# Kernel tuning notes

Measured on AMD Instinct MI355X. Metric: run time of the kernel, lower is better.

## Reference

```python
import jax, jax.numpy as jnp
import numpy as np

N_NODES = 100000
N_EDGES = 1600000
IN_SIZE = 128
HIDDEN = 32
OUT_SIZE = 16


def _mean_agg(h, src, dst, n_nodes):
    # segment-sum of source features into destination nodes, then divide by in-degree
    summed = jax.ops.segment_sum(h[src], dst, num_segments=n_nodes)  # [N, D]
    deg = jax.ops.segment_sum(jnp.ones((src.shape[0],), h.dtype), dst, num_segments=n_nodes)
    return summed / jnp.maximum(deg, 1.0)[:, None]


def _sage_layer(h, src, dst, W_self, W_neigh, b):
    # DGL SAGEConv (mean): fc_self(h) + fc_neigh(mean_neigh(h)) + bias
    agg = _mean_agg(h, src, dst, h.shape[0])
    return h @ W_self + agg @ W_neigh + b


def setup_inputs() -> dict:
    key = jax.random.key(0)
    ks = jax.random.split(key, 9)
    inp = {
        "x": jax.random.normal(ks[0], (N_NODES, IN_SIZE), jnp.float32),
        "edge_src": jax.random.randint(ks[1], (N_EDGES,), 0, N_NODES, jnp.int32),
        "edge_dst": jax.random.randint(ks[2], (N_EDGES,), 0, N_NODES, jnp.int32),
        "W_self1": jax.random.normal(ks[3], (IN_SIZE, HIDDEN), jnp.float32) / np.sqrt(IN_SIZE),
        "W_neigh1": jax.random.normal(ks[4], (IN_SIZE, HIDDEN), jnp.float32) / np.sqrt(IN_SIZE),
        "b1": jnp.zeros((HIDDEN,), jnp.float32),
        "W_self2": jax.random.normal(ks[5], (HIDDEN, HIDDEN), jnp.float32) / np.sqrt(HIDDEN),
        "W_neigh2": jax.random.normal(ks[6], (HIDDEN, HIDDEN), jnp.float32) / np.sqrt(HIDDEN),
        "b2": jnp.zeros((HIDDEN,), jnp.float32),
        "W_self3": jax.random.normal(ks[7], (HIDDEN, OUT_SIZE), jnp.float32) / np.sqrt(HIDDEN),
        "W_neigh3": jax.random.normal(ks[8], (HIDDEN, OUT_SIZE), jnp.float32) / np.sqrt(HIDDEN),
        "b3": jnp.zeros((OUT_SIZE,), jnp.float32),
    }
    return inp


def reference(x, edge_src, edge_dst,
              W_self1, W_neigh1, b1,
              W_self2, W_neigh2, b2,
              W_self3, W_neigh3, b3):
    h = jax.nn.relu(_sage_layer(x, edge_src, edge_dst, W_self1, W_neigh1, b1))
    h = jax.nn.relu(_sage_layer(h, edge_src, edge_dst, W_self2, W_neigh2, b2))
    h = _sage_layer(h, edge_src, edge_dst, W_self3, W_neigh3, b3)
    return h
```

## Files before the change

### kernel.cpp

```cpp
#include <hip/hip_runtime.h>


#define BLOCK 256
#define NBLK 256
#define BSH 9
#define CAP 12288

__global__ void hist_kernel(const int* __restrict__ dst, int* __restrict__ hist,
                            int n_edges, int nbuk, int ch) {
    __shared__ int cnt[256];
    int tid = threadIdx.x;
    for (int i = tid; i < nbuk; i += BLOCK) cnt[i] = 0;
    __syncthreads();
    int e0 = blockIdx.x * ch;
    int e1 = e0 + ch; if (e1 > n_edges) e1 = n_edges;
    for (int e = e0 + tid; e < e1; e += BLOCK)
        atomicAdd(&cnt[dst[e] >> BSH], 1);
    __syncthreads();
    for (int i = tid; i < nbuk; i += BLOCK)
        hist[i * NBLK + blockIdx.x] = cnt[i];
}

__global__ void scanBlk_kernel(int* __restrict__ hist, int* __restrict__ buktot) {
    int b = blockIdx.x;
    int tid = threadIdx.x;
    int orig = hist[b * NBLK + tid];
    int v = orig;
    int lane = tid & 63, w = tid >> 6;
#pragma unroll
    for (int off = 1; off < 64; off <<= 1) {
        int u = __shfl_up(v, off);
        if (lane >= off) v += u;
    }
    __shared__ int wps[4];
    if (lane == 63) wps[w] = v;
    __syncthreads();
    int wadd = 0;
    for (int k = 0; k < w; ++k) wadd += wps[k];
    int excl = v - orig + wadd;
    hist[b * NBLK + tid] = excl;
    if (tid == 255) buktot[b] = excl + orig;
}

__global__ void scanBuk_kernel(const int* __restrict__ buktot, int* __restrict__ bukoff,
                               int nbuk, int* __restrict__ startp, int n_nodes, int n_edges) {
    int tid = threadIdx.x;
    int orig = (tid < nbuk) ? buktot[tid] : 0;
    int v = orig;
    int lane = tid & 63, w = tid >> 6;
#pragma unroll
    for (int off = 1; off < 64; off <<= 1) {
        int u = __shfl_up(v, off);
        if (lane >= off) v += u;
    }
    __shared__ int wps[4];
    if (lane == 63) wps[w] = v;
    __syncthreads();
    int wadd = 0;
    for (int k = 0; k < w; ++k) wadd += wps[k];
    int excl = v - orig + wadd;
    if (tid < nbuk) bukoff[tid] = excl;
    if (tid == 0) { bukoff[nbuk] = n_edges; startp[n_nodes] = n_edges; }
}

__global__ void part_kernel(const int* __restrict__ src, const int* __restrict__ dst,
                            const int* __restrict__ hist, const int* __restrict__ bukoff,
                            int2* __restrict__ pairs, int n_edges, int nbuk, int ch) {
    __shared__ int base[256];
    __shared__ int cnt[256];
    int tid = threadIdx.x;
    for (int i = tid; i < nbuk; i += BLOCK) {
        base[i] = hist[i * NBLK + blockIdx.x] + bukoff[i];
        cnt[i] = 0;
    }
    __syncthreads();
    int e0 = blockIdx.x * ch;
    int e1 = e0 + ch; if (e1 > n_edges) e1 = n_edges;
    for (int e = e0 + tid; e < e1; e += BLOCK) {
        int d = dst[e];
        int b = d >> BSH;
        int r = atomicAdd(&cnt[b], 1);
        pairs[base[b] + r] = make_int2(src[e], d);
    }
}

__global__ void build_kernel(const int2* __restrict__ pairs, const int* __restrict__ bukoff,
                             int* __restrict__ start, float* __restrict__ invdeg,
                             int* __restrict__ csr_src, int n_nodes) {
    __shared__ int deg[512];
    __shared__ int lst[512];
    __shared__ int cur[512];
    __shared__ int wps[4];
    __shared__ int scsr[CAP];

    int b = blockIdx.x;
    int tid = threadIdx.x;
    int e0 = bukoff[b];
    int e1 = bukoff[b + 1];
    int lo = b << BSH;
    int hi = lo + (1 << BSH); if (hi > n_nodes) hi = n_nodes;
    int nn = hi - lo;
    int ne = e1 - e0;

    for (int i = tid; i < 512; i += BLOCK) deg[i] = 0;
    __syncthreads();
    for (int i = e0 + tid; i < e1; i += BLOCK)
        atomicAdd(&deg[pairs[i].y - lo], 1);
    __syncthreads();

    int d0 = deg[2 * tid], d1 = deg[2 * tid + 1];
    int s = d0 + d1;
    int lane = tid & 63, w = tid >> 6;
    int v = s;
#pragma unroll
    for (int off = 1; off < 64; off <<= 1) {
        int u = __shfl_up(v, off);
        if (lane >= off) v += u;
    }
    if (lane == 63) wps[w] = v;
    __syncthreads();
    int wb = 0;
    for (int k = 0; k < w; ++k) wb += wps[k];
    int excl = wb + v - s;
    lst[2 * tid] = excl;
    lst[2 * tid + 1] = excl + d0;
    cur[2 * tid] = 0;
    cur[2 * tid + 1] = 0;
    __syncthreads();

    for (int i = tid; i < nn; i += BLOCK) {
        start[lo + i] = e0 + lst[i];
        int d = deg[i];
        invdeg[lo + i] = 1.0f / (float)(d < 1 ? 1 : d);
    }

    if (ne <= CAP) {
        for (int i = e0 + tid; i < e1; i += BLOCK) {
            int2 pr = pairs[i];
            int dl = pr.y - lo;
            int sl = lst[dl] + atomicAdd(&cur[dl], 1);
            scsr[sl] = pr.x;
        }
        __syncthreads();
        for (int i = tid; i < ne; i += BLOCK) csr_src[e0 + i] = scsr[i];
    } else {
        for (int i = e0 + tid; i < e1; i += BLOCK) {
            int2 pr = pairs[i];
            int dl = pr.y - lo;
            int sl = lst[dl] + atomicAdd(&cur[dl], 1);
            csr_src[e0 + sl] = pr.x;
        }
    }
}

template<int DIN, int DOUT, int OPT, int NPT>
__global__ __launch_bounds__(256, 4)
void proj_reg(const float* __restrict__ h,
              const float* __restrict__ Ws,
              const float* __restrict__ Wn,
              const float* __restrict__ bias,
              float* __restrict__ pre,
              float* __restrict__ p,
              int n_nodes) {
    constexpr int OD  = 2 * DOUT;
    constexpr int OG  = OD / OPT;
    constexpr int NG  = 256 / OG;
    constexpr int NT  = NPT * NG;
    constexpr int NV  = OPT / 4;

    __shared__ float sW[DIN][OD];
    __shared__ float sb[DOUT];

    const int tid = threadIdx.x;
    for (int i = tid; i < DIN * OD; i += 256) {
        int k = i / OD, o = i % OD;
        sW[k][o] = (o < DOUT) ? Ws[k * DOUT + o] : Wn[k * DOUT + (o - DOUT)];
    }
    if (tid < DOUT) sb[tid] = bias[tid];
    __syncthreads();

    const int to = tid % OG;
    const int tn = tid / OG;
    const int o0 = to * OPT;
    const int node0 = blockIdx.x * NT + tn * NPT;

    const float4* __restrict__ xp[NPT];
#pragma unroll
    for (int n = 0; n < NPT; ++n) {
        int node = node0 + n;
        int safe = (node < n_nodes) ? node : (n_nodes - 1);
        xp[n] = reinterpret_cast<const float4*>(h + (size_t)safe * DIN);
    }

    float acc[NPT][OPT];
#pragma unroll
    for (int n = 0; n < NPT; ++n)
#pragma unroll
        for (int o = 0; o < OPT; ++o) acc[n][o] = 0.f;

#pragma unroll 2
    for (int k4 = 0; k4 < DIN / 4; ++k4) {
        float4 xv[NPT];
#pragma unroll
        for (int n = 0; n < NPT; ++n) xv[n] = xp[n][k4];
#pragma unroll
        for (int kk = 0; kk < 4; ++kk) {
            int k = 4 * k4 + kk;
            float4 w[NV];
#pragma unroll
            for (int v = 0; v < NV; ++v)
                w[v] = *reinterpret_cast<const float4*>(&sW[k][o0 + 4 * v]);
#pragma unroll
            for (int n = 0; n < NPT; ++n) {
                float xk = reinterpret_cast<const float*>(&xv[n])[kk];
#pragma unroll
                for (int v = 0; v < NV; ++v) {
                    acc[n][4 * v + 0] = fmaf(xk, w[v].x, acc[n][4 * v + 0]);
                    acc[n][4 * v + 1] = fmaf(xk, w[v].y, acc[n][4 * v + 1]);
                    acc[n][4 * v + 2] = fmaf(xk, w[v].z, acc[n][4 * v + 2]);
                    acc[n][4 * v + 3] = fmaf(xk, w[v].w, acc[n][4 * v + 3]);
                }
            }
        }
    }

    const bool self_half = (o0 < DOUT);
    const int oo = self_half ? o0 : (o0 - DOUT);
    float* __restrict__ dstbuf = self_half ? pre : p;
#pragma unroll
    for (int n = 0; n < NPT; ++n) {
        int node = node0 + n;
        if (node >= n_nodes) continue;
#pragma unroll
        for (int v = 0; v < NV; ++v) {
            float4 r;
            r.x = acc[n][4 * v + 0];
            r.y = acc[n][4 * v + 1];
            r.z = acc[n][4 * v + 2];
            r.w = acc[n][4 * v + 3];
            if (self_half) {
                r.x += sb[oo + 4 * v + 0];
                r.y += sb[oo + 4 * v + 1];
                r.z += sb[oo + 4 * v + 2];
                r.w += sb[oo + 4 * v + 3];
            }
            *reinterpret_cast<float4*>(dstbuf + (size_t)node * DOUT + oo + 4 * v) = r;
        }
    }
}

template<int D, bool RELU>
__global__ void gather_kernel(const float* __restrict__ p,
                              const int* __restrict__ csr_src,
                              const int* __restrict__ start,
                              const float* __restrict__ pre,
                              const float* __restrict__ invdeg,
                              float* __restrict__ out,
                              int n_nodes) {
    constexpr int LPN = D / 4;
    constexpr int NPG = 64 / LPN;
    int wave = threadIdx.x >> 6;
    int lane = threadIdx.x & 63;
    int g = blockIdx.x * (blockDim.x >> 6) + wave;
    if (g >= n_nodes) return;
    int sub = lane / LPN;
    int fl  = lane % LPN;
    int s0 = start[g];
    int s1 = start[g + 1];
    const float4* __restrict__ p4 = reinterpret_cast<const float4*>(p);
    float4 a0 = make_float4(0.f, 0.f, 0.f, 0.f);
    float4 a1 = make_float4(0.f, 0.f, 0.f, 0.f);
    int j = s0 + sub;
    for (; j + NPG < s1; j += 2 * NPG) {
        int c0 = csr_src[j];
        int c1 = csr_src[j + NPG];
        float4 v0 = p4[c0 * LPN + fl];
        float4 v1 = p4[c1 * LPN + fl];
        a0.x += v0.x; a0.y += v0.y; a0.z += v0.z; a0.w += v0.w;
        a1.x += v1.x; a1.y += v1.y; a1.z += v1.z; a1.w += v1.w;
    }
    if (j < s1) {
        float4 v = p4[csr_src[j] * LPN + fl];
        a0.x += v.x; a0.y += v.y; a0.z += v.z; a0.w += v.w;
    }
    float4 a = make_float4(a0.x + a1.x, a0.y + a1.y, a0.z + a1.z, a0.w + a1.w);
#pragma unroll
    for (int off = 32; off >= LPN; off >>= 1) {
        a.x += __shfl_down(a.x, off);
        a.y += __shfl_down(a.y, off);
        a.z += __shfl_down(a.z, off);
        a.w += __shfl_down(a.w, off);
    }
    if (lane < LPN) {
        float id = invdeg[g];
        float4 pr = reinterpret_cast<const float4*>(pre)[g * LPN + fl];
        float4 r;
        r.x = pr.x + a.x * id;
        r.y = pr.y + a.y * id;
        r.z = pr.z + a.z * id;
        r.w = pr.w + a.w * id;
        if (RELU) {
            r.x = fmaxf(r.x, 0.f); r.y = fmaxf(r.y, 0.f);
            r.z = fmaxf(r.z, 0.f); r.w = fmaxf(r.w, 0.f);
        }
        reinterpret_cast<float4*>(out)[g * LPN + fl] = r;
    }
}

extern "C" void kernel_launch(void* const* d_in, const int* in_sizes, int n_in,
                              void* d_out, int out_size, void* d_ws, size_t ws_size,
                              hipStream_t stream) {
    const float* x        = (const float*)d_in[0];
    const int*   edge_src = (const int*)d_in[1];
    const int*   edge_dst = (const int*)d_in[2];
    const float* Ws1 = (const float*)d_in[3];
    const float* Wn1 = (const float*)d_in[4];
    const float* b1  = (const float*)d_in[5];
    const float* Ws2 = (const float*)d_in[6];
    const float* Wn2 = (const float*)d_in[7];
    const float* b2  = (const float*)d_in[8];
    const float* Ws3 = (const float*)d_in[9];
    const float* Wn3 = (const float*)d_in[10];
    const float* b3  = (const float*)d_in[11];
    float* out = (float*)d_out;

    const int IN = 128, HID = 32;
    const int n_nodes = in_sizes[0] / IN;
    const int n_edges = in_sizes[1];
    const int nbuk = (n_nodes + (1 << BSH) - 1) >> BSH;
    const int ch   = (n_edges + NBLK - 1) / NBLK;

    char* wsb = (char*)d_ws;
    size_t off = 0;
    auto alloc = [&](size_t bytes) { char* r = wsb + off; off = (off + bytes + 255) & ~(size_t)255; return r; };
    int*   startp = (int*)alloc(((size_t)n_nodes + 1) * sizeof(int));
    float* invdeg = (float*)alloc((size_t)n_nodes * sizeof(float));
    int*   csr    = (int*)alloc((size_t)n_edges * sizeof(int));
    int*   hist   = (int*)alloc((size_t)nbuk * NBLK * sizeof(int));
    int*   buktot = (int*)alloc(256 * sizeof(int));
    int*   bukoff = (int*)alloc(257 * sizeof(int));
    float* B0     = (float*)alloc((size_t)n_nodes * HID * sizeof(float));
    float* B1     = (float*)alloc((size_t)n_nodes * HID * sizeof(float));
    float* B3     = (float*)alloc((size_t)n_nodes * HID * sizeof(float));
    int2*  pairs  = (int2*)B0;

    const int gP    = (n_nodes + 63) / 64;
    const int gGat  = (n_nodes + 3) / 4;

    hist_kernel   <<<NBLK, BLOCK, 0, stream>>>(edge_dst, hist, n_edges, nbuk, ch);
    scanBlk_kernel<<<nbuk, BLOCK, 0, stream>>>(hist, buktot);
    scanBuk_kernel<<<1, BLOCK, 0, stream>>>(buktot, bukoff, nbuk, startp, n_nodes, n_edges);
    part_kernel   <<<NBLK, BLOCK, 0, stream>>>(edge_src, edge_dst, hist, bukoff, pairs, n_edges, nbuk, ch);
    build_kernel  <<<nbuk, BLOCK, 0, stream>>>(pairs, bukoff, startp, invdeg, csr, n_nodes);

    proj_reg<128, 32, 8, 2><<<gP, BLOCK, 0, stream>>>(x, Ws1, Wn1, b1, B0, B1, n_nodes);
    gather_kernel<32, true><<<gGat, BLOCK, 0, stream>>>(B1, csr, startp, B0, invdeg, B3, n_nodes);

    proj_reg<32, 32, 8, 2><<<gP, BLOCK, 0, stream>>>(B3, Ws2, Wn2, b2, B0, B1, n_nodes);
    gather_kernel<32, true><<<gGat, BLOCK, 0, stream>>>(B1, csr, startp, B0, invdeg, B3, n_nodes);

    proj_reg<32, 16, 4, 2><<<gP, BLOCK, 0, stream>>>(B3, Ws3, Wn3, b3, B0, B1, n_nodes);
    gather_kernel<16, false><<<gGat, BLOCK, 0, stream>>>(B1, csr, startp, B0, invdeg, out, n_nodes);
}
```

Measured before the change: 216.9 us.

## Pack edge pairs into 32-bit words and restructure gather to lane-per-feature

Edge (src, local dst) pairs are packed into a single 32-bit word (20-bit src, local dst in the upper bits), halving partition-buffer traffic between the partition and CSR build kernels. The gather kernel is rewritten so each lane owns one feature of one node and walks the whole neighbour list with 8 independent scalar accumulators, removing the cross-lane shuffle reduction. The projection inner loop is also manually unrolled by two k-steps to load two weight rows at once. The packing assumes node ids fit in 20 bits and the local dst in 12, and the scalar gather loads fewer bytes per instruction than the old float4 path.

```diff
diff --git a/kernel.cpp b/kernel.cpp
--- a/kernel.cpp
+++ b/kernel.cpp
@@ -65,7 +65,7 @@
 
 __global__ void part_kernel(const int* __restrict__ src, const int* __restrict__ dst,
                             const int* __restrict__ hist, const int* __restrict__ bukoff,
-                            int2* __restrict__ pairs, int n_edges, int nbuk, int ch) {
+                            unsigned* __restrict__ pairs, int n_edges, int nbuk, int ch) {
     __shared__ int base[256];
     __shared__ int cnt[256];
     int tid = threadIdx.x;
@@ -79,12 +79,13 @@
     for (int e = e0 + tid; e < e1; e += BLOCK) {
         int d = dst[e];
         int b = d >> BSH;
+        unsigned dl = (unsigned)(d & ((1 << BSH) - 1));
         int r = atomicAdd(&cnt[b], 1);
-        pairs[base[b] + r] = make_int2(src[e], d);
-    }
-}
-
-__global__ void build_kernel(const int2* __restrict__ pairs, const int* __restrict__ bukoff,
+        pairs[base[b] + r] = (unsigned)src[e] | (dl << 20);
+    }
+}
+
+__global__ void build_kernel(const unsigned* __restrict__ pairs, const int* __restrict__ bukoff,
                              int* __restrict__ start, float* __restrict__ invdeg,
                              int* __restrict__ csr_src, int n_nodes) {
     __shared__ int deg[512];
@@ -105,7 +106,7 @@
     for (int i = tid; i < 512; i += BLOCK) deg[i] = 0;
     __syncthreads();
     for (int i = e0 + tid; i < e1; i += BLOCK)
-        atomicAdd(&deg[pairs[i].y - lo], 1);
+        atomicAdd(&deg[pairs[i] >> 20], 1);
     __syncthreads();
 
     int d0 = deg[2 * tid], d1 = deg[2 * tid + 1];
@@ -136,19 +137,19 @@
 
     if (ne <= CAP) {
         for (int i = e0 + tid; i < e1; i += BLOCK) {
-            int2 pr = pairs[i];
-            int dl = pr.y - lo;
+            unsigned pr = pairs[i];
+            int dl = pr >> 20;
             int sl = lst[dl] + atomicAdd(&cur[dl], 1);
-            scsr[sl] = pr.x;
+            scsr[sl] = (int)(pr & 0xFFFFFu);
         }
         __syncthreads();
         for (int i = tid; i < ne; i += BLOCK) csr_src[e0 + i] = scsr[i];
     } else {
         for (int i = e0 + tid; i < e1; i += BLOCK) {
-            int2 pr = pairs[i];
-            int dl = pr.y - lo;
+            unsigned pr = pairs[i];
+            int dl = pr >> 20;
             int sl = lst[dl] + atomicAdd(&cur[dl], 1);
-            csr_src[e0 + sl] = pr.x;
+            csr_src[e0 + sl] = (int)(pr & 0xFFFFFu);
         }
     }
 }
@@ -204,21 +205,34 @@
 #pragma unroll
         for (int n = 0; n < NPT; ++n) xv[n] = xp[n][k4];
 #pragma unroll
-        for (int kk = 0; kk < 4; ++kk) {
+        for (int kk = 0; kk < 4; kk += 2) {
             int k = 4 * k4 + kk;
-            float4 w[NV];
-#pragma unroll
-            for (int v = 0; v < NV; ++v)
-                w[v] = *reinterpret_cast<const float4*>(&sW[k][o0 + 4 * v]);
+            float4 w0[NV], w1[NV];
+#pragma unroll
+            for (int v = 0; v < NV; ++v) {
+                w0[v] = *reinterpret_cast<const float4*>(&sW[k][o0 + 4 * v]);
+                w1[v] = *reinterpret_cast<const float4*>(&sW[k + 1][o0 + 4 * v]);
+            }
 #pragma unroll
             for (int n = 0; n < NPT; ++n) {
                 float xk = reinterpret_cast<const float*>(&xv[n])[kk];
 #pragma unroll
                 for (int v = 0; v < NV; ++v) {
-                    acc[n][4 * v + 0] = fmaf(xk, w[v].x, acc[n][4 * v + 0]);
-                    acc[n][4 * v + 1] = fmaf(xk, w[v].y, acc[n][4 * v + 1]);
-                    acc[n][4 * v + 2] = fmaf(xk, w[v].z, acc[n][4 * v + 2]);
-                    acc[n][4 * v + 3] = fmaf(xk, w[v].w, acc[n][4 * v + 3]);
+                    acc[n][4 * v + 0] = fmaf(xk, w0[v].x, acc[n][4 * v + 0]);
+                    acc[n][4 * v + 1] = fmaf(xk, w0[v].y, acc[n][4 * v + 1]);
+                    acc[n][4 * v + 2] = fmaf(xk, w0[v].z, acc[n][4 * v + 2]);
+                    acc[n][4 * v + 3] = fmaf(xk, w0[v].w, acc[n][4 * v + 3]);
+                }
+            }
+#pragma unroll
+            for (int n = 0; n < NPT; ++n) {
+                float xk = reinterpret_cast<const float*>(&xv[n])[kk + 1];
+#pragma unroll
+                for (int v = 0; v < NV; ++v) {
+                    acc[n][4 * v + 0] = fmaf(xk, w1[v].x, acc[n][4 * v + 0]);
+                    acc[n][4 * v + 1] = fmaf(xk, w1[v].y, acc[n][4 * v + 1]);
+                    acc[n][4 * v + 2] = fmaf(xk, w1[v].z, acc[n][4 * v + 2]);
+                    acc[n][4 * v + 3] = fmaf(xk, w1[v].w, acc[n][4 * v + 3]);
                 }
             }
         }
@@ -257,54 +271,42 @@
                               const float* __restrict__ invdeg,
                               float* __restrict__ out,
                               int n_nodes) {
-    constexpr int LPN = D / 4;
-    constexpr int NPG = 64 / LPN;
+    constexpr int NPW = 64 / D;
     int wave = threadIdx.x >> 6;
     int lane = threadIdx.x & 63;
-    int g = blockIdx.x * (blockDim.x >> 6) + wave;
+    int g = (blockIdx.x * (blockDim.x >> 6) + wave) * NPW + lane / D;
+    int f = lane % D;
     if (g >= n_nodes) return;
-    int sub = lane / LPN;
-    int fl  = lane % LPN;
     int s0 = start[g];
     int s1 = start[g + 1];
-    const float4* __restrict__ p4 = reinterpret_cast<const float4*>(p);
-    float4 a0 = make_float4(0.f, 0.f, 0.f, 0.f);
-    float4 a1 = make_float4(0.f, 0.f, 0.f, 0.f);
-    int j = s0 + sub;
-    for (; j + NPG < s1; j += 2 * NPG) {
-        int c0 = csr_src[j];
-        int c1 = csr_src[j + NPG];
-        float4 v0 = p4[c0 * LPN + fl];
-        float4 v1 = p4[c1 * LPN + fl];
-        a0.x += v0.x; a0.y += v0.y; a0.z += v0.z; a0.w += v0.w;
-        a1.x += v1.x; a1.y += v1.y; a1.z += v1.z; a1.w += v1.w;
-    }
-    if (j < s1) {
-        float4 v = p4[csr_src[j] * LPN + fl];
-        a0.x += v.x; a0.y += v.y; a0.z += v.z; a0.w += v.w;
-    }
-    float4 a = make_float4(a0.x + a1.x, a0.y + a1.y, a0.z + a1.z, a0.w + a1.w);
-#pragma unroll
-    for (int off = 32; off >= LPN; off >>= 1) {
-        a.x += __shfl_down(a.x, off);
-        a.y += __shfl_down(a.y, off);
-        a.z += __shfl_down(a.z, off);
-        a.w += __shfl_down(a.w, off);
-    }
-    if (lane < LPN) {
-        float id = invdeg[g];
-        float4 pr = reinterpret_cast<const float4*>(pre)[g * LPN + fl];
-        float4 r;
-        r.x = pr.x + a.x * id;
-        r.y = pr.y + a.y * id;
-        r.z = pr.z + a.z * id;
-        r.w = pr.w + a.w * id;
-        if (RELU) {
-            r.x = fmaxf(r.x, 0.f); r.y = fmaxf(r.y, 0.f);
-            r.z = fmaxf(r.z, 0.f); r.w = fmaxf(r.w, 0.f);
-        }
-        reinterpret_cast<float4*>(out)[g * LPN + fl] = r;
-    }
+    float a0 = 0.f, a1 = 0.f, a2 = 0.f, a3 = 0.f;
+    float a4 = 0.f, a5 = 0.f, a6 = 0.f, a7 = 0.f;
+    int j = s0;
+    for (; j + 8 <= s1; j += 8) {
+        int c0 = csr_src[j + 0], c1 = csr_src[j + 1];
+        int c2 = csr_src[j + 2], c3 = csr_src[j + 3];
+        int c4 = csr_src[j + 4], c5 = csr_src[j + 5];
+        int c6 = csr_src[j + 6], c7 = csr_src[j + 7];
+        a0 += p[(size_t)c0 * D + f];
+        a1 += p[(size_t)c1 * D + f];
+        a2 += p[(size_t)c2 * D + f];
+        a3 += p[(size_t)c3 * D + f];
+        a4 += p[(size_t)c4 * D + f];
+        a5 += p[(size_t)c5 * D + f];
+        a6 += p[(size_t)c6 * D + f];
+        a7 += p[(size_t)c7 * D + f];
+    }
+    for (; j + 2 <= s1; j += 2) {
+        int c0 = csr_src[j], c1 = csr_src[j + 1];
+        a0 += p[(size_t)c0 * D + f];
+        a1 += p[(size_t)c1 * D + f];
+    }
+    if (j < s1) a2 += p[(size_t)csr_src[j] * D + f];
+    float a = ((a0 + a1) + (a2 + a3)) + ((a4 + a5) + (a6 + a7));
+    size_t o = (size_t)g * D + f;
+    float v = pre[o] + a * invdeg[g];
+    if (RELU) v = fmaxf(v, 0.f);
+    out[o] = v;
 }
 
 extern "C" void kernel_launch(void* const* d_in, const int* in_sizes, int n_in,
@@ -342,10 +344,11 @@
     float* B0     = (float*)alloc((size_t)n_nodes * HID * sizeof(float));
     float* B1     = (float*)alloc((size_t)n_nodes * HID * sizeof(float));
     float* B3     = (float*)alloc((size_t)n_nodes * HID * sizeof(float));
-    int2*  pairs  = (int2*)B0;
-
-    const int gP    = (n_nodes + 63) / 64;
-    const int gGat  = (n_nodes + 3) / 4;
+    unsigned* pairs = (unsigned*)B0;
+
+    const int gP     = (n_nodes + 63) / 64;
+    const int gGat32 = (n_nodes + 7) / 8;
+    const int gGat16 = (n_nodes + 15) / 16;
 
     hist_kernel   <<<NBLK, BLOCK, 0, stream>>>(edge_dst, hist, n_edges, nbuk, ch);
     scanBlk_kernel<<<nbuk, BLOCK, 0, stream>>>(hist, buktot);
@@ -354,11 +357,11 @@
     build_kernel  <<<nbuk, BLOCK, 0, stream>>>(pairs, bukoff, startp, invdeg, csr, n_nodes);
 
     proj_reg<128, 32, 8, 2><<<gP, BLOCK, 0, stream>>>(x, Ws1, Wn1, b1, B0, B1, n_nodes);
-    gather_kernel<32, true><<<gGat, BLOCK, 0, stream>>>(B1, csr, startp, B0, invdeg, B3, n_nodes);
+    gather_kernel<32, true><<<gGat32, BLOCK, 0, stream>>>(B1, csr, startp, B0, invdeg, B3, n_nodes);
 
     proj_reg<32, 32, 8, 2><<<gP, BLOCK, 0, stream>>>(B3, Ws2, Wn2, b2, B0, B1, n_nodes);
-    gather_kernel<32, true><<<gGat, BLOCK, 0, stream>>>(B1, csr, startp, B0, invdeg, B3, n_nodes);
+    gather_kernel<32, true><<<gGat32, BLOCK, 0, stream>>>(B1, csr, startp, B0, invdeg, B3, n_nodes);
 
     proj_reg<32, 16, 4, 2><<<gP, BLOCK, 0, stream>>>(B3, Ws3, Wn3, b3, B0, B1, n_nodes);
-    gather_kernel<16, false><<<gGat, BLOCK, 0, stream>>>(B1, csr, startp, B0, invdeg, out, n_nodes);
-}
+    gather_kernel<16, false><<<gGat16, BLOCK, 0, stream>>>(B1, csr, startp, B0, invdeg, out, n_nodes);
+}
```

New measurement: 205.0 us. -5.5%, faster.
